# Kernel tuning notes

Measured on AMD Instinct MI355X. Metric: run time of the kernel, lower is better.

The kernel has to match this reference:

```python
import jax, jax.numpy as jnp
import numpy as np

SMOOTH = 1e-6
ALPHA = 0.25
GAMMA = 2.0
W_DICE, W_CLDICE, W_FOCAL = 0.1, 0.7, 0.2


def _shift(x, dy, dx):
    # x: [B,H,W]; value of neighbor at (i+dy, j+dx), zero-padded borders
    H, W = x.shape[1], x.shape[2]
    p = jnp.pad(x, ((0, 0), (1, 1), (1, 1)))
    return p[:, 1 + dy:1 + dy + H, 1 + dx:1 + dx + W]


def _thin_subiter(img, sub):
    # One Zhang-Suen thinning sub-iteration (matches skimage 2D skeletonize algorithm).
    p2 = _shift(img, -1, 0)   # N
    p3 = _shift(img, -1, 1)   # NE
    p4 = _shift(img, 0, 1)    # E
    p5 = _shift(img, 1, 1)    # SE
    p6 = _shift(img, 1, 0)    # S
    p7 = _shift(img, 1, -1)   # SW
    p8 = _shift(img, 0, -1)   # W
    p9 = _shift(img, -1, -1)  # NW
    nbrs = [p2, p3, p4, p5, p6, p7, p8, p9]
    B = sum(nbrs)
    # A = number of 0->1 transitions in circular sequence p2..p9
    A = sum(((nbrs[k] < 0.5) & (nbrs[(k + 1) % 8] > 0.5)).astype(jnp.int32)
            for k in range(8))
    c1 = (B >= 2.0) & (B <= 6.0)
    c2 = (A == 1)
    if sub == 0:
        c3 = (p2 * p4 * p6) == 0.0
        c4 = (p4 * p6 * p8) == 0.0
    else:
        c3 = (p2 * p4 * p8) == 0.0
        c4 = (p2 * p6 * p8) == 0.0
    remove = (img > 0.5) & c1 & c2 & c3 & c4
    return jnp.where(remove, 0.0, img)


def _skeletonize(img):
    # img: [B,H,W] float32 in {0,1}. Iterate thinning to convergence.
    def body(state):
        cur, _ = state
        new = _thin_subiter(_thin_subiter(cur, 0), 1)
        return (new, jnp.any(new != cur))

    out, _ = jax.lax.while_loop(lambda s: s[1], body, (img, jnp.array(True)))
    return out


def setup_inputs() -> dict:
    key = jax.random.key(0)
    k1, k2 = jax.random.split(key)
    logits = jax.random.normal(k1, (16, 2, 512, 512), dtype=jnp.float32)
    true = jax.random.randint(k2, (16, 512, 512), 0, 2, dtype=jnp.int32)
    return {"logits": logits, "true": true}


def reference(logits, true):
    probs = jax.nn.softmax(logits, axis=1)

    # --- clDice (detached in torch original -> stop_gradient, non-differentiable) ---
    pred = jax.lax.stop_gradient(probs[:, 1])          # [B,H,W]
    pred_bin = (pred > 0.5).astype(jnp.float32)
    true_bin = (true > 0).astype(jnp.float32)
    pred_skel = _skeletonize(pred_bin)
    true_skel = _skeletonize(true_bin)
    inter = jnp.sum(pred_skel * true_skel, axis=(1, 2))
    denom = jnp.sum(pred_skel, axis=(1, 2)) + jnp.sum(true_skel, axis=(1, 2))
    cldice = (2.0 * inter + SMOOTH) / (denom + SMOOTH)
    cldice_loss = 1.0 - jnp.mean(cldice)

    # --- Dice ---
    n_cls = probs.shape[1]
    t1h = jax.nn.one_hot(true, n_cls, axis=1, dtype=probs.dtype)  # [B,C,H,W]
    inter_d = jnp.sum(probs * t1h, axis=(0, 2, 3))
    card = jnp.sum(probs + t1h, axis=(0, 2, 3))
    dice_loss = 1.0 - jnp.mean((2.0 * inter_d + SMOOTH) / (card + SMOOTH))

    # --- Focal ---
    logp = jax.nn.log_softmax(logits, axis=1)
    ce = -jnp.take_along_axis(logp, true[:, None, :, :].astype(jnp.int32), axis=1)[:, 0]
    pt = jnp.exp(-ce)
    focal_loss = jnp.mean(ALPHA * (1.0 - pt) ** GAMMA * ce)

    return W_CLDICE * cldice_loss + W_DICE * dice_loss + W_FOCAL * focal_loss
```

## Files before the change

### kernel.cpp

```cpp
#include <hip/hip_runtime.h>
#include <hip/hip_bf16.h>

typedef unsigned long long u64;

#define NB 16
#define HW 512
#define PIX_PER_B (HW * HW)
#define NPIX (NB * PIX_PER_B)
#define WORDS_PER_B (PIX_PER_B / 64)
#define SROW 9

#define WS_PART_OFF 1024
#define WS_MASK_OFF 32768
#define WS_NEED_MASKS (WS_MASK_OFF + (size_t)2 * NB * WORDS_PER_B * 8)

#define RED_BLOCKS 224
#define FB_BLOCKS 512
#define MASK_BLOCKS 2048



__device__ __forceinline__ void fa3(u64 a, u64 b, u64 c, u64& s, u64& cy) {
  u64 x = a ^ b;
  s = x ^ c;
  cy = (a & b) | (c & x);
}

__device__ __forceinline__ u64 thin_word(u64 nm, u64 nl, u64 nr,
                                         u64 cm, u64 cl, u64 cr,
                                         u64 sm, u64 sl, u64 sr, int sub) {
  u64 p2 = nm;
  u64 p3 = (nm >> 1) | (nr << 63);
  u64 p4 = (cm >> 1) | (cr << 63);
  u64 p5 = (sm >> 1) | (sr << 63);
  u64 p6 = sm;
  u64 p7 = (sm << 1) | (sl >> 63);
  u64 p8 = (cm << 1) | (cl >> 63);
  u64 p9 = (nm << 1) | (nl >> 63);

  u64 u1, v1, u2, v2, ss, sc, cs, cc;
  fa3(p2, p3, p4, u1, v1);
  fa3(p5, p6, p7, u2, v2);
  u64 u3 = p8 ^ p9, v3 = p8 & p9;
  fa3(u1, u2, u3, ss, sc);
  fa3(v1, v2, v3, cs, cc);
  u64 w  = sc & cs;
  u64 b1 = sc ^ cs;
  u64 b2 = cc ^ w;
  u64 b3 = cc & w;
  u64 cond1 = (sc | cs | cc) & ~(b3 | (b2 & b1 & ss));

  u64 t0 = ~p2 & p3, t1 = ~p3 & p4, t2 = ~p4 & p5, t3 = ~p5 & p6;
  u64 t4 = ~p6 & p7, t5 = ~p7 & p8, t6 = ~p8 & p9, t7 = ~p9 & p2;
  u64 as1, ac1, as2, ac2, Ass, Asc, Acs, Acc;
  fa3(t0, t1, t2, as1, ac1);
  fa3(t3, t4, t5, as2, ac2);
  u64 as3 = t6 ^ t7, ac3 = t6 & t7;
  fa3(as1, as2, as3, Ass, Asc);
  fa3(ac1, ac2, ac3, Acs, Acc);
  u64 cond2 = Ass & ~(Asc | Acs | Acc);

  u64 cond3, cond4;
  if (sub == 0) { cond3 = ~(p2 & p4 & p6); cond4 = ~(p4 & p6 & p8); }
  else          { cond3 = ~(p2 & p4 & p8); cond4 = ~(p2 & p6 & p8); }

  u64 rem = cm & cond1 & cond2 & cond3 & cond4;
  return cm & ~rem;
}


__global__ __launch_bounds__(256) void mask_kernel(
    const float* __restrict__ logits, const int* __restrict__ tr,
    unsigned char* __restrict__ ws) {
  int tid = threadIdx.x, blk = blockIdx.x;
  int lane = tid & 63;
  u64* predM = (u64*)(ws + WS_MASK_OFF);
  u64* trueM = predM + (size_t)NB * WORDS_PER_B;
  if (blk == 0 && tid < 64) ((u64*)(ws + 64))[tid] = 0;

  int wv = (blk * 256 + tid) >> 6;
#pragma unroll
  for (int it = 0; it < 2; ++it) {
    int T = wv * 2 + it;
    int P = T << 8;
    int b = P >> 18;
    int rbase = (P & (PIX_PER_B - 1)) + lane;
    const float* lp0 = logits + (size_t)b * 2 * PIX_PER_B;
    const float* lp1 = lp0 + PIX_PER_B;
    const int* tp = tr + (size_t)b * PIX_PER_B;
    float l0v[4], l1v[4];
    int tv[4];
#pragma unroll
    for (int k = 0; k < 4; k++) {
      int r = rbase + k * 64;
      l0v[k] = lp0[r];
      l1v[k] = lp1[r];
      tv[k] = tp[r];
    }
    u64 pw[4], twd[4];
#pragma unroll
    for (int k = 0; k < 4; k++) {
      pw[k] = __ballot(l1v[k] > l0v[k]);
      twd[k] = __ballot(tv[k] > 0);
    }
    if (lane == 0) {
#pragma unroll
      for (int k = 0; k < 4; k++) {
        predM[T * 4 + k] = pw[k];
        trueM[T * 4 + k] = twd[k];
      }
    }
  }
}


__global__ __launch_bounds__(1024) void fused_kernel(
    const float* __restrict__ logits, const int* __restrict__ tr,
    unsigned char* __restrict__ ws) {
  __shared__ u64 S[HW * SROW];
  __shared__ unsigned char dirty[2][130];
  __shared__ int flag;
  __shared__ double red[16][6];

  int tid  = threadIdx.x;
  int lane = tid & 63;

  if (blockIdx.x < 32) {
    int b    = blockIdx.x;
    int img  = b & 15;
    int wcol = tid & 7;
    int s    = tid >> 3;
    int r0   = s * 4;

    u64* region = (u64*)(ws + WS_MASK_OFF) + (size_t)b * WORDS_PER_B;
    u64* clInter = (u64*)(ws + 64);
    u64* clSp    = (u64*)(ws + 192);
    u64* clSt    = (u64*)(ws + 320);
    u64* done    = (u64*)(ws + 448);

#pragma unroll
    for (int i = 0; i < 4; i++)
      S[(r0 + i) * SROW + wcol] = region[(r0 + i) * 8 + wcol];
    if (tid < 130) {
      unsigned char init = (tid >= 1 && tid <= 128) ? 1 : 0;
      dirty[0][tid] = init;
      dirty[1][tid] = init;
    }
    if (tid == 0) flag = 0;
    __syncthreads();

    auto loadRow = [&](int r, u64& m, u64& l, u64& rr) {
      if (r < 0 || r >= HW) { m = 0; l = 0; rr = 0; return; }
      const u64* row = &S[r * SROW];
      m  = row[wcol];
      l  = wcol ? row[wcol - 1] : 0ULL;
      rr = (wcol < 7) ? row[wcol + 1] : 0ULL;
    };

    auto subIter = [&](int sub, int db, int pairTag) {
      unsigned char* dOut = dirty[db ^ 1];
      bool laneActive = (dirty[0][s] | dirty[0][s + 1] | dirty[0][s + 2] |
                         dirty[1][s] | dirty[1][s + 1] | dirty[1][s + 2]) != 0;
      u64 wmask = __ballot(laneActive);
      bool stripCh = false;
      u64 nw[4];
      bool doit = (wmask != 0);
      if (doit) {
        u64 am, al, ar, bm, bl, br, cmv, clv, crv, oldc[4];
        loadRow(r0 - 1, am, al, ar);
        loadRow(r0,     bm, bl, br);
#pragma unroll
        for (int i = 0; i < 4; i++) {
          loadRow(r0 + 1 + i, cmv, clv, crv);
          oldc[i] = bm;
          nw[i] = thin_word(am, al, ar, bm, bl, br, cmv, clv, crv, sub);
          am = bm; al = bl; ar = br;
          bm = cmv; bl = clv; br = crv;
        }
        bool ch = false;
#pragma unroll
        for (int i = 0; i < 4; i++) ch |= (nw[i] != oldc[i]);
        u64 bal = __ballot(ch);
        stripCh = ((bal >> (lane & 56)) & 0xFFULL) != 0;
      }
      __syncthreads();
      if (doit) {
#pragma unroll
        for (int i = 0; i < 4; i++) S[(r0 + i) * SROW + wcol] = nw[i];
      }
      if ((tid & 7) == 0) {
        dOut[s + 1] = stripCh ? 1 : 0;
        if (stripCh) flag = pairTag;
      }
      __syncthreads();
    };

    for (int pair = 1; pair <= 2000; ++pair) {
      subIter(0, 0, pair);
      subIter(1, 1, pair);
      if (flag != pair) break;
    }

    u64 own[4];
    u64 cnt = 0;
#pragma unroll
    for (int i = 0; i < 4; i++) {
      own[i] = S[(r0 + i) * SROW + wcol];
      cnt += (u64)__popcll(own[i]);
    }
    for (int o = 32; o; o >>= 1) cnt += __shfl_down(cnt, o, 64);

    if (b < NB) {
#pragma unroll
      for (int i = 0; i < 4; i++) region[(r0 + i) * 8 + wcol] = own[i];
      if (lane == 0) atomicAdd(clSp + img, cnt);
      __syncthreads();
      if (tid == 0) {
        __threadfence();
        __hip_atomic_store(&done[img], 1ULL, __ATOMIC_RELEASE, __HIP_MEMORY_SCOPE_AGENT);
      }
    } else {
      if (lane == 0) atomicAdd(clSt + img, cnt);
      if (tid == 0) {
        while (__hip_atomic_load(&done[img], __ATOMIC_ACQUIRE,
                                 __HIP_MEMORY_SCOPE_AGENT) == 0ULL) {
          __builtin_amdgcn_s_sleep(8);
        }
        __threadfence();
      }
      __syncthreads();
      const u64* predRegion = (const u64*)(ws + WS_MASK_OFF) + (size_t)img * WORDS_PER_B;
      u64 inL = 0;
#pragma unroll
      for (int i = 0; i < 4; i++) {
        u64 pw = __hip_atomic_load(&predRegion[(r0 + i) * 8 + wcol],
                                   __ATOMIC_RELAXED, __HIP_MEMORY_SCOPE_AGENT);
        inL += (u64)__popcll(pw & own[i]);
      }
      for (int o = 32; o; o >>= 1) inL += __shfl_down(inL, o, 64);
      if (lane == 0) atomicAdd(clInter + img, inL);
    }

  } else {
    int rb = blockIdx.x - 32;
    double a0 = 0, a1 = 0, s0 = 0, s1 = 0, cnt = 0, fo = 0;
    for (int g = rb * 1024 + tid; g < NPIX; g += RED_BLOCKS * 1024) {
      int b = g >> 18;
      int r = g & (PIX_PER_B - 1);
      const float* lp = logits + (size_t)b * 2 * PIX_PER_B + r;
      float l0 = lp[0], l1 = lp[PIX_PER_B];
      int t = tr[g];
      float m = fmaxf(l0, l1);
      float e0 = expf(l0 - m), e1 = expf(l1 - m);
      float ssum = e0 + e1;
      float p0 = e0 / ssum, p1 = e1 / ssum;
      if (t) a1 += (double)p1; else a0 += (double)p0;
      s0 += (double)p0;
      s1 += (double)p1;
      cnt += (double)t;
      float lse = m + logf(ssum);
      float ce = lse - (t ? l1 : l0);
      float pt = t ? p1 : p0;
      float om = 1.0f - pt;
      fo += (double)(0.25f * om * om * ce);
    }
    double v[6] = {a0, a1, s0, s1, cnt, fo};
    int wv = tid >> 6;
#pragma unroll
    for (int j = 0; j < 6; j++) {
      double x = v[j];
      for (int o = 32; o; o >>= 1) x += __shfl_down(x, o, 64);
      if (lane == 0) red[wv][j] = x;
    }
    __syncthreads();
    if (tid < 6) {
      double t6 = 0;
      for (int w = 0; w < 16; w++) t6 += red[w][tid];
      double* part = (double*)(ws + WS_PART_OFF) + (size_t)rb * 6;
      part[tid] = t6;
    }
  }
}


__global__ __launch_bounds__(512) void finalize_kernel(unsigned char* __restrict__ ws,
                                                       float* __restrict__ out, int count) {
  int tid = threadIdx.x;
  const double* part = (const double*)(ws + WS_PART_OFF);
  double v[6] = {0, 0, 0, 0, 0, 0};
  if (tid < count) {
#pragma unroll
    for (int j = 0; j < 6; j++) v[j] = part[(size_t)tid * 6 + j];
  }
  __shared__ double red[8][6];
  int lane = tid & 63, wv = tid >> 6;
#pragma unroll
  for (int j = 0; j < 6; j++) {
    double x = v[j];
    for (int o = 32; o; o >>= 1) x += __shfl_down(x, o, 64);
    if (lane == 0) red[wv][j] = x;
  }
  __syncthreads();
  if (tid == 0) {
    double t[6] = {0, 0, 0, 0, 0, 0};
    for (int w = 0; w < 8; w++)
      for (int j = 0; j < 6; j++) t[j] += red[w][j];
    double a0 = t[0], a1 = t[1], s0 = t[2], s1 = t[3], cnt = t[4], fo = t[5];

    const double N = (double)NPIX;
    double cnt0 = N - cnt;
    double card0 = s0 + cnt0, card1 = s1 + cnt;
    double dice = 0.5 * ((2.0 * a0 + 1e-6) / (card0 + 1e-6) +
                         (2.0 * a1 + 1e-6) / (card1 + 1e-6));
    double diceL = 1.0 - dice;
    double focalL = fo / N;

    const u64* clInter = (const u64*)(ws + 64);
    const u64* clSp    = (const u64*)(ws + 192);
    const u64* clSt    = (const u64*)(ws + 320);
    double cs = 0;
    for (int b = 0; b < NB; b++) {
      double inter = (double)clInter[b];
      double den = (double)(clSp[b] + clSt[b]);
      cs += (2.0 * inter + 1e-6) / (den + 1e-6);
    }
    double clL = 1.0 - cs / (double)NB;

    out[0] = (float)(0.7 * clL + 0.1 * diceL + 0.2 * focalL);
  }
}


__global__ __launch_bounds__(256) void loss_reduce_fb_kernel(
    const float* __restrict__ logits, const int* __restrict__ tr,
    unsigned char* __restrict__ ws) {
  int tid = threadIdx.x;
  double a0 = 0, a1 = 0, s0 = 0, s1 = 0, cnt = 0, fo = 0;
  const int iters = NPIX / (FB_BLOCKS * 256);
  for (int it = 0; it < iters; ++it) {
    int g = (it * FB_BLOCKS + (int)blockIdx.x) * 256 + tid;
    int b = g >> 18;
    int r = g & (PIX_PER_B - 1);
    const float* lp = logits + (size_t)b * 2 * PIX_PER_B + r;
    float l0 = lp[0], l1 = lp[PIX_PER_B];
    int t = tr[g];
    float m = fmaxf(l0, l1);
    float e0 = expf(l0 - m), e1 = expf(l1 - m);
    float s = e0 + e1;
    float p0 = e0 / s, p1 = e1 / s;
    if (t) a1 += (double)p1; else a0 += (double)p0;
    s0 += (double)p0;
    s1 += (double)p1;
    cnt += (double)t;
    float lse = m + logf(s);
    float ce = lse - (t ? l1 : l0);
    float pt = t ? p1 : p0;
    float om = 1.0f - pt;
    fo += (double)(0.25f * om * om * ce);
  }
  __shared__ double red[4][6];
  double v[6] = {a0, a1, s0, s1, cnt, fo};
  int lane = tid & 63, wv = tid >> 6;
#pragma unroll
  for (int j = 0; j < 6; j++) {
    double x = v[j];
    for (int o = 32; o; o >>= 1) x += __shfl_down(x, o, 64);
    if (lane == 0) red[wv][j] = x;
  }
  __syncthreads();
  if (tid < 6) {
    double* part = (double*)(ws + WS_PART_OFF) + (size_t)blockIdx.x * 6;
    part[tid] = red[0][tid] + red[1][tid] + red[2][tid] + red[3][tid];
  }
}

__global__ __launch_bounds__(1024) void skel_combined_kernel(
    const float* __restrict__ logits, const int* __restrict__ tr,
    unsigned char* __restrict__ ws) {
  __shared__ u64 S[HW * SROW];
  __shared__ int flag;

  int tid  = threadIdx.x;
  int b    = blockIdx.x;
  int wcol = tid & 7;
  int r0   = (tid >> 3) * 4;
  int lane = tid & 63;

  u64* clInter = (u64*)(ws + 64);
  u64* clSp    = (u64*)(ws + 192);
  u64* clSt    = (u64*)(ws + 320);

  auto buildPred = [&]() {
    const float* lp0 = logits + (size_t)b * 2 * PIX_PER_B;
    const float* lp1 = lp0 + PIX_PER_B;
    for (int k = 0; k < PIX_PER_B / 1024; k++) {
      int p = k * 1024 + tid;
      u64 msk = __ballot(lp1[p] > lp0[p]);
      if (lane == 0) { int wi = p >> 6; S[(wi >> 3) * SROW + (wi & 7)] = msk; }
    }
    __syncthreads();
  };
  auto buildTrue = [&]() {
    const int* tp = tr + (size_t)b * PIX_PER_B;
    for (int k = 0; k < PIX_PER_B / 1024; k++) {
      int p = k * 1024 + tid;
      u64 msk = __ballot(tp[p] > 0);
      if (lane == 0) { int wi = p >> 6; S[(wi >> 3) * SROW + (wi & 7)] = msk; }
    }
    __syncthreads();
  };

  auto loadRow = [&](int r, u64& m, u64& l, u64& rr) {
    if (r < 0 || r >= HW) { m = 0; l = 0; rr = 0; return; }
    const u64* row = &S[r * SROW];
    m  = row[wcol];
    l  = wcol ? row[wcol - 1] : 0ULL;
    rr = (wcol < 7) ? row[wcol + 1] : 0ULL;
  };

  auto subIter = [&](int sub) {
    u64 am, al, ar, bm, bl, br, cmv, clv, crv;
    u64 nw[4], oldc[4];
    loadRow(r0 - 1, am, al, ar);
    loadRow(r0,     bm, bl, br);
#pragma unroll
    for (int i = 0; i < 4; i++) {
      loadRow(r0 + 1 + i, cmv, clv, crv);
      oldc[i] = bm;
      nw[i] = thin_word(am, al, ar, bm, bl, br, cmv, clv, crv, sub);
      am = bm; al = bl; ar = br;
      bm = cmv; bl = clv; br = crv;
    }
    __syncthreads();
    bool ch = false;
#pragma unroll
    for (int i = 0; i < 4; i++) {
      S[(r0 + i) * SROW + wcol] = nw[i];
      ch |= (nw[i] != oldc[i]);
    }
    if (ch) flag = 1;
    __syncthreads();
  };

  auto thinConverge = [&]() {
    for (int it = 0; it < 2000; ++it) {
      if (tid == 0) flag = 0;
      __syncthreads();
      subIter(0);
      subIter(1);
      int f = flag;
      __syncthreads();
      if (!f) break;
    }
  };

  buildPred();
  thinConverge();
  u64 pr[4];
  u64 spL = 0;
#pragma unroll
  for (int i = 0; i < 4; i++) {
    pr[i] = S[(r0 + i) * SROW + wcol];
    spL += (u64)__popcll(pr[i]);
  }
  __syncthreads();

  buildTrue();
  thinConverge();
  u64 stL = 0, inL = 0;
#pragma unroll
  for (int i = 0; i < 4; i++) {
    u64 tw = S[(r0 + i) * SROW + wcol];
    stL += (u64)__popcll(tw);
    inL += (u64)__popcll(tw & pr[i]);
  }

  for (int o = 32; o; o >>= 1) {
    spL += __shfl_down(spL, o, 64);
    stL += __shfl_down(stL, o, 64);
    inL += __shfl_down(inL, o, 64);
  }
  if (lane == 0) {
    atomicAdd(clSp + b, spL);
    atomicAdd(clSt + b, stL);
    atomicAdd(clInter + b, inL);
  }
}


extern "C" void kernel_launch(void* const* d_in, const int* in_sizes, int n_in,
                              void* d_out, int out_size, void* d_ws, size_t ws_size,
                              hipStream_t stream) {
  const float* logits = (const float*)d_in[0];
  const int* tr = (const int*)d_in[1];
  float* out = (float*)d_out;
  unsigned char* ws = (unsigned char*)d_ws;

  if (ws_size >= WS_NEED_MASKS) {
    hipLaunchKernelGGL(mask_kernel, dim3(MASK_BLOCKS), dim3(256), 0, stream,
                       logits, tr, ws);
    hipLaunchKernelGGL(fused_kernel, dim3(32 + RED_BLOCKS), dim3(1024), 0, stream,
                       logits, tr, ws);
    hipLaunchKernelGGL(finalize_kernel, dim3(1), dim3(512), 0, stream, ws, out, RED_BLOCKS);
  } else {
    hipMemsetAsync(d_ws, 0, 512, stream);
    hipLaunchKernelGGL(loss_reduce_fb_kernel, dim3(FB_BLOCKS), dim3(256), 0, stream,
                       logits, tr, ws);
    hipLaunchKernelGGL(skel_combined_kernel, dim3(NB), dim3(1024), 0, stream,
                       logits, tr, ws);
    hipLaunchKernelGGL(finalize_kernel, dim3(1), dim3(512), 0, stream, ws, out, FB_BLOCKS);
  }
}
```

Baseline: 126.7 us.

## Double-buffer skeleton thinning in shared memory to drop one barrier per sub-iteration

The Zhang-Suen thinning loop now ping-pongs between two shared-memory bitmaps. Each sub-iteration can read one buffer and write the other without waiting on a barrier between the compute and write phases, so it needs one __syncthreads instead of two. The dirty-strip tracking becomes a 3-slot ring and the convergence flag a 4-slot ring, so the two preceding sub-iterations can be checked without a race. The cost is twice the shared memory for the bitmap, and inactive strips rely on the stale buffer copy matching the current state.

```diff
diff --git a/kernel.cpp b/kernel.cpp
--- a/kernel.cpp
+++ b/kernel.cpp
@@ -17,7 +17,6 @@
 #define RED_BLOCKS 224
 #define FB_BLOCKS 512
 #define MASK_BLOCKS 2048
-
 
 
 __device__ __forceinline__ void fa3(u64 a, u64 b, u64 c, u64& s, u64& cy) {
@@ -117,9 +116,9 @@
 __global__ __launch_bounds__(1024) void fused_kernel(
     const float* __restrict__ logits, const int* __restrict__ tr,
     unsigned char* __restrict__ ws) {
-  __shared__ u64 S[HW * SROW];
-  __shared__ unsigned char dirty[2][130];
-  __shared__ int flag;
+  __shared__ u64 SB[2][HW * SROW];
+  __shared__ unsigned char dirt[3][130];
+  __shared__ int flagRing[4];
   __shared__ double red[16][6];
 
   int tid  = threadIdx.x;
@@ -140,72 +139,71 @@
 
 #pragma unroll
     for (int i = 0; i < 4; i++)
-      S[(r0 + i) * SROW + wcol] = region[(r0 + i) * 8 + wcol];
+      SB[0][(r0 + i) * SROW + wcol] = region[(r0 + i) * 8 + wcol];
     if (tid < 130) {
       unsigned char init = (tid >= 1 && tid <= 128) ? 1 : 0;
-      dirty[0][tid] = init;
-      dirty[1][tid] = init;
-    }
-    if (tid == 0) flag = 0;
+      dirt[0][tid] = init;
+      dirt[1][tid] = init;
+      dirt[2][tid] = init;
+    }
+    if (tid < 4) flagRing[tid] = 0;
     __syncthreads();
 
-    auto loadRow = [&](int r, u64& m, u64& l, u64& rr) {
+    auto loadRow = [&](const u64* B, int r, u64& m, u64& l, u64& rr) {
       if (r < 0 || r >= HW) { m = 0; l = 0; rr = 0; return; }
-      const u64* row = &S[r * SROW];
+      const u64* row = B + r * SROW;
       m  = row[wcol];
       l  = wcol ? row[wcol - 1] : 0ULL;
       rr = (wcol < 7) ? row[wcol + 1] : 0ULL;
     };
 
-    auto subIter = [&](int sub, int db, int pairTag) {
-      unsigned char* dOut = dirty[db ^ 1];
-      bool laneActive = (dirty[0][s] | dirty[0][s + 1] | dirty[0][s + 2] |
-                         dirty[1][s] | dirty[1][s + 1] | dirty[1][s + 2]) != 0;
-      u64 wmask = __ballot(laneActive);
-      bool stripCh = false;
-      u64 nw[4];
-      bool doit = (wmask != 0);
-      if (doit) {
-        u64 am, al, ar, bm, bl, br, cmv, clv, crv, oldc[4];
-        loadRow(r0 - 1, am, al, ar);
-        loadRow(r0,     bm, bl, br);
-#pragma unroll
-        for (int i = 0; i < 4; i++) {
-          loadRow(r0 + 1 + i, cmv, clv, crv);
-          oldc[i] = bm;
-          nw[i] = thin_word(am, al, ar, bm, bl, br, cmv, clv, crv, sub);
-          am = bm; al = bl; ar = br;
-          bm = cmv; bl = clv; br = crv;
+    int t = 0;
+    bool conv = false;
+    for (int p = 0; p < 1024 && !conv; ++p) {
+      for (int sub = 0; sub < 2; ++sub, ++t) {
+        int wslot = t % 3;
+        int g1 = (t + 2) % 3;
+        int g2 = (t + 1) % 3;
+        const u64* src = SB[t & 1];
+        u64* dst = SB[(t & 1) ^ 1];
+        bool laneActive = (dirt[g1][s] | dirt[g1][s + 1] | dirt[g1][s + 2] |
+                           dirt[g2][s] | dirt[g2][s + 1] | dirt[g2][s + 2]) != 0;
+        u64 wmask = __ballot(laneActive);
+        bool doit = (wmask != 0);
+        bool stripCh = false;
+        if (doit) {
+          u64 am, al, ar, bm, bl, br, cmv, clv, crv, nw[4];
+          loadRow(src, r0 - 1, am, al, ar);
+          loadRow(src, r0,     bm, bl, br);
+          bool ch = false;
+#pragma unroll
+          for (int i = 0; i < 4; i++) {
+            loadRow(src, r0 + 1 + i, cmv, clv, crv);
+            nw[i] = thin_word(am, al, ar, bm, bl, br, cmv, clv, crv, sub);
+            ch |= (nw[i] != bm);
+            am = bm; al = bl; ar = br;
+            bm = cmv; bl = clv; br = crv;
+          }
+          u64 bal = __ballot(ch);
+          stripCh = ((bal >> (lane & 56)) & 0xFFULL) != 0;
+#pragma unroll
+          for (int i = 0; i < 4; i++) dst[(r0 + i) * SROW + wcol] = nw[i];
         }
-        bool ch = false;
-#pragma unroll
-        for (int i = 0; i < 4; i++) ch |= (nw[i] != oldc[i]);
-        u64 bal = __ballot(ch);
-        stripCh = ((bal >> (lane & 56)) & 0xFFULL) != 0;
+        if ((tid & 7) == 0) {
+          dirt[wslot][s + 1] = stripCh ? 1 : 0;
+          if (stripCh) flagRing[p & 3] = 1;
+        }
+        if (sub == 0 && tid == 0) flagRing[(p + 2) & 3] = 0;
+        __syncthreads();
       }
-      __syncthreads();
-      if (doit) {
-#pragma unroll
-        for (int i = 0; i < 4; i++) S[(r0 + i) * SROW + wcol] = nw[i];
-      }
-      if ((tid & 7) == 0) {
-        dOut[s + 1] = stripCh ? 1 : 0;
-        if (stripCh) flag = pairTag;
-      }
-      __syncthreads();
-    };
-
-    for (int pair = 1; pair <= 2000; ++pair) {
-      subIter(0, 0, pair);
-      subIter(1, 1, pair);
-      if (flag != pair) break;
+      if (flagRing[p & 3] == 0) conv = true;
     }
 
     u64 own[4];
     u64 cnt = 0;
 #pragma unroll
     for (int i = 0; i < 4; i++) {
-      own[i] = S[(r0 + i) * SROW + wcol];
+      own[i] = SB[0][(r0 + i) * SROW + wcol];
       cnt += (u64)__popcll(own[i]);
     }
     for (int o = 32; o; o >>= 1) cnt += __shfl_down(cnt, o, 64);
```

New measurement: 129.4 us. 2.2% more time.
